# Optimization experiments

Hardware: AMD Instinct MI355X
Metric: run time of the kernel (lower is better)

## Reference

```python
import jax, jax.numpy as jnp
import numpy as np

NEG_SLOPE = 0.2

def gat_conv(x, edge_index, W, a_src, a_dst, b):
    # PyG GATConv, heads=1, eval mode (dropout off), add_self_loops=True
    N = x.shape[0]
    h = x @ W                                   # [N, C]
    loops = jnp.arange(N, dtype=edge_index.dtype)
    src = jnp.concatenate([edge_index[0], loops])
    dst = jnp.concatenate([edge_index[1], loops])
    s_src = h @ a_src                            # [N]
    s_dst = h @ a_dst                            # [N]
    e = s_src[src] + s_dst[dst]                  # [E+N]
    e = jnp.where(e > 0, e, NEG_SLOPE * e)       # leaky_relu
    # segment softmax over destination neighborhoods
    m = jax.ops.segment_max(e, dst, num_segments=N)
    ex = jnp.exp(e - m[dst])
    denom = jax.ops.segment_sum(ex, dst, num_segments=N)
    alpha = ex / denom[dst]                      # [E+N]
    out = jax.ops.segment_sum(alpha[:, None] * h[src], dst, num_segments=N)
    return out + b

def setup_inputs() -> dict:
    key = jax.random.key(0)
    ks = jax.random.split(key, 10)
    N, F_in, H, C, E = 100000, 256, 128, 40, 1600000
    x = jax.random.normal(ks[0], (N, F_in), dtype=jnp.float32)
    edge_index = jax.random.randint(ks[1], (2, E), 0, N, dtype=jnp.int64)
    s1 = 1.0 / np.sqrt(F_in)
    s2 = 1.0 / np.sqrt(H)
    W1 = jax.random.normal(ks[2], (F_in, H), dtype=jnp.float32) * s1
    a_src1 = jax.random.normal(ks[3], (H,), dtype=jnp.float32) * s2
    a_dst1 = jax.random.normal(ks[4], (H,), dtype=jnp.float32) * s2
    b1 = jnp.zeros((H,), dtype=jnp.float32)
    W2 = jax.random.normal(ks[5], (H, C), dtype=jnp.float32) * s2
    a_src2 = jax.random.normal(ks[6], (C,), dtype=jnp.float32) * 0.1
    a_dst2 = jax.random.normal(ks[7], (C,), dtype=jnp.float32) * 0.1
    b2 = jnp.zeros((C,), dtype=jnp.float32)
    return {"x": x, "edge_index": edge_index, "W1": W1, "a_src1": a_src1,
            "a_dst1": a_dst1, "b1": b1, "W2": W2, "a_src2": a_src2,
            "a_dst2": a_dst2, "b2": b2}

def reference(x, edge_index, W1, a_src1, a_dst1, b1, W2, a_src2, a_dst2, b2):
    h = gat_conv(x, edge_index, W1, a_src1, a_dst1, b1)
    h = jax.nn.relu(h)
    # dropout(p=0.6) is identity in eval mode
    h = gat_conv(h, edge_index, W2, a_src2, a_dst2, b2)
    return jax.nn.log_softmax(h, axis=1)
```

## Files before the change

### kernel.cpp

```cpp
#include <hip/hip_runtime.h>
#include <math.h>

#define NEG_SLOPE 0.2f
#define CAP 64
#define NB 64
#define NBUCKET 1563
#define BCAP 1408
#define BINCHUNK 8192
#define NBINB 196

typedef __attribute__((ext_vector_type(8))) short short8;
typedef __attribute__((ext_vector_type(4))) short short4v;
typedef __attribute__((ext_vector_type(4))) float f32x4;
typedef __attribute__((ext_vector_type(2))) float f32x2;

__device__ inline unsigned short f2bf(float f) {
    union { float f; unsigned u; } x; x.f = f;
    unsigned r = x.u + 0x7FFFu + ((x.u >> 16) & 1u);
    return (unsigned short)(r >> 16);
}

__device__ __forceinline__ void gload_lds16(const void* g, void* l) {
    __builtin_amdgcn_global_load_lds(
        (const __attribute__((address_space(1))) void*)g,
        (__attribute__((address_space(3))) void*)l, 16, 0, 0);
}


__global__ __launch_bounds__(256) void init_kernel(
    const float* __restrict__ W1, const float* __restrict__ W2,
    short* __restrict__ bsw1, short* __restrict__ bsw2,
    int* __restrict__ ctrl)
{
    int t = blockIdx.x * 256 + threadIdx.x;
    if (t < 4096) {
        int lane = t & 63;
        int f = t >> 6;
        int k_step = f & 7;
        int n_tile = f >> 3;
        int n  = n_tile * 16 + (lane & 15);
        int k0 = k_step * 32 + (lane >> 4) * 8;
        short8 v;
        #pragma unroll
        for (int j = 0; j < 8; j++)
            v[j] = (short)f2bf(W1[(size_t)(k0 + j) * 128 + n]);
        ((short8*)bsw1)[t] = v;
    } else if (t < 4096 + 768) {
        int u = t - 4096;
        int lane = u & 63;
        int f = u >> 6;
        int k_step = f & 3;
        int n_tile = f >> 2;
        int n  = n_tile * 16 + (lane & 15);
        int k0 = k_step * 32 + (lane >> 4) * 8;
        short8 v;
        #pragma unroll
        for (int j = 0; j < 8; j++)
            v[j] = (n < 40) ? (short)f2bf(W2[(size_t)(k0 + j) * 40 + n]) : (short)0;
        ((short8*)bsw2)[u] = v;
    } else {
        for (int i = t - 4864; i < NBUCKET + 4; i += 256)
            if (i >= 0) ctrl[i] = 0;
    }
}

__global__ __launch_bounds__(256, 2) void k1_kernel(
    const int* __restrict__ ei, int* __restrict__ bcnt,
    unsigned* __restrict__ bbuf, int E,
    const float* __restrict__ x, const short* __restrict__ bsw,
    const float* __restrict__ a_src, const float* __restrict__ a_dst,
    unsigned char* __restrict__ h1, float* __restrict__ s_src,
    float* __restrict__ s_dst, int M)
{
    __shared__ __align__(16) char smem[16896];
    const int tid = threadIdx.x;
    const int bi = blockIdx.x;
    const int q = bi / 9, r = bi - q * 9;

    if (r == 0 && q < NBINB) {
        int* lc = (int*)smem;
        const int base = q * BINCHUNK;
        int n = E - base; if (n > BINCHUNK) n = BINCHUNK;

        for (int b = tid; b < NBUCKET; b += 256) lc[b] = 0;
        __syncthreads();
        for (int i = tid; i < n; i += 256)
            atomicAdd(&lc[ei[E + base + i] >> 6], 1);
        __syncthreads();
        for (int b = tid; b < NBUCKET; b += 256) {
            int c = lc[b];
            lc[b] = c ? atomicAdd(&bcnt[b], c) : 0;
        }
        __syncthreads();
        for (int i = tid; i < n; i += 256) {
            int s = ei[base + i];
            int d = ei[E + base + i];
            int b = d >> 6;
            int pos = atomicAdd(&lc[b], 1);
            if (pos < BCAP)
                bbuf[(size_t)b * BCAP + pos] = (unsigned)s | ((unsigned)(d & 63) << 17);
        }
        return;
    }

    const int nbin = (q < NBINB) ? (q + (r ? 1 : 0)) : NBINB;
    const int vb = bi - nbin;
    const int wave = tid >> 6, lane = tid & 63;
    short8* lbs = (short8*)smem;
    const int rowBase = vb * 64;
    const int arow = rowBase + wave * 16 + (lane & 15);
    const int acol0 = (lane >> 4) * 8;
    const bool rv = (arow < M);
    const float* __restrict__ xr = x + (size_t)arow * 256 + acol0;
    const char* __restrict__ bsb = (const char*)bsw;

    auto stage = [&](int buf, int nt) {
        const char* s = bsb + nt * 8192 + wave * 2048 + lane * 16;
        char* d = smem + buf * 8192 + wave * 2048 + lane * 16;
        gload_lds16(s, d);
        gload_lds16(s + 1024, d + 1024);
    };

    stage(0, 0);

    float4 px[8], qx[8];
    #pragma unroll
    for (int k = 0; k < 8; k++) {
        px[k] = make_float4(0.f, 0.f, 0.f, 0.f);
        qx[k] = px[k];
        if (rv) {
            px[k] = *(const float4*)(xr + k * 32);
            qx[k] = *(const float4*)(xr + k * 32 + 4);
        }
    }
    short8 a[8];
    #pragma unroll
    for (int k = 0; k < 8; k++) {
        short8 t;
        t[0] = (short)f2bf(px[k].x); t[1] = (short)f2bf(px[k].y);
        t[2] = (short)f2bf(px[k].z); t[3] = (short)f2bf(px[k].w);
        t[4] = (short)f2bf(qx[k].x); t[5] = (short)f2bf(qx[k].y);
        t[6] = (short)f2bf(qx[k].z); t[7] = (short)f2bf(qx[k].w);
        a[k] = t;
    }

    const int R0 = rowBase + wave * 16 + (lane >> 4) * 4;
    const int Cb = lane & 15;

    float asv[8], adv[8];
    #pragma unroll
    for (int nt = 0; nt < 8; nt++) {
        asv[nt] = a_src[nt * 16 + Cb];
        adv[nt] = a_dst[nt * 16 + Cb];
    }

    stage(1, 1);

    float ss[4] = {0.f, 0.f, 0.f, 0.f};
    float sd[4] = {0.f, 0.f, 0.f, 0.f};
    f32x4 prev = {0.f, 0.f, 0.f, 0.f};
    int wpk[4][4];

    #pragma unroll
    for (int nt = 0; nt < 8; nt++) {
        if (nt == 7) asm volatile("s_waitcnt vmcnt(0)" ::: "memory");
        else         asm volatile("s_waitcnt vmcnt(2)" ::: "memory");
        __builtin_amdgcn_s_barrier();

        short8 breg[8];
        #pragma unroll
        for (int k = 0; k < 8; k++) breg[k] = lbs[(nt & 1) * 512 + k * 64 + lane];
        asm volatile("s_waitcnt lgkmcnt(0)" ::: "memory");
        __builtin_amdgcn_sched_barrier(0);
        __builtin_amdgcn_s_barrier();

        if (nt < 6) stage(nt & 1, nt + 2);

        __builtin_amdgcn_s_setprio(1);
        f32x4 acc = {0.f, 0.f, 0.f, 0.f};
        #pragma unroll
        for (int k = 0; k < 8; k++)
            acc = __builtin_amdgcn_mfma_f32_16x16x32_bf16(a[k], breg[k], acc, 0, 0, 0);
        __builtin_amdgcn_s_setprio(0);

        float as_ = asv[nt], ad_ = adv[nt];
        #pragma unroll
        for (int r2 = 0; r2 < 4; r2++) {
            float v = acc[r2];
            ss[r2] = fmaf(v, as_, ss[r2]);
            sd[r2] = fmaf(v, ad_, sd[r2]);
        }
        if (nt & 1) {
            #pragma unroll
            for (int r2 = 0; r2 < 4; r2++)
                wpk[nt >> 1][r2] = __builtin_amdgcn_cvt_pk_fp8_f32(prev[r2], acc[r2], 0, false);
        } else {
            prev = acc;
        }
    }

    #pragma unroll
    for (int r2 = 0; r2 < 4; r2++) {
        int R = R0 + r2;
        if (R < M) {
            #pragma unroll
            for (int t = 0; t < 4; t++)
                *(unsigned short*)(h1 + (size_t)R * 128 + t * 32 + 2 * Cb) =
                    (unsigned short)wpk[t][r2];
        }
    }
    #pragma unroll
    for (int off = 1; off < 16; off <<= 1) {
        #pragma unroll
        for (int r2 = 0; r2 < 4; r2++) {
            ss[r2] += __shfl_xor(ss[r2], off);
            sd[r2] += __shfl_xor(sd[r2], off);
        }
    }
    if ((lane & 15) == 0) {
        #pragma unroll
        for (int r2 = 0; r2 < 4; r2++) {
            int R = R0 + r2;
            if (R < M) { s_src[R] = ss[r2]; s_dst[R] = sd[r2]; }
        }
    }
}

__global__ __launch_bounds__(256) void fill_kernel(
    const int* __restrict__ bcnt, const unsigned* __restrict__ bbuf,
    int* __restrict__ csr, int* __restrict__ sorted, int* __restrict__ clsCnt,
    int M)
{
    __shared__ int lcnt[NB];
    __shared__ int lcsr[NB][CAP];
    __shared__ int chist[4];
    __shared__ int cbase[4];
    const int tid = threadIdx.x;
    const int b = blockIdx.x;
    const int nb = b * NB;

    if (tid < NB) lcnt[tid] = 0;
    if (tid < 4) chist[tid] = 0;
    __syncthreads();

    if (tid < NB && nb + tid < M) {
        int pos = atomicAdd(&lcnt[tid], 1);
        if (pos < CAP) lcsr[tid][pos] = nb + tid;
    }

    int ne = bcnt[b]; if (ne > BCAP) ne = BCAP;
    const unsigned* __restrict__ bp = bbuf + (size_t)b * BCAP;
    for (int j = tid; j < ne; j += 256) {
        unsigned v = bp[j];
        int s  = v & 0x1FFFF;
        int dl = v >> 17;
        int pos = atomicAdd(&lcnt[dl], 1);
        if (pos < CAP) lcsr[dl][pos] = s;
    }
    __syncthreads();

    const int4* __restrict__ srcp = (const int4*)&lcsr[0][0];
    int4* __restrict__ dstp = (int4*)(csr + (size_t)nb * CAP);
    #pragma unroll 4
    for (int j = tid; j < NB * CAP / 4; j += 256) dstp[j] = srcp[j];

    int deg = 0, cls = 0, pos = 0;
    bool isNode = (tid < NB && nb + tid < M);
    if (isNode) {
        deg = lcnt[tid]; if (deg > CAP) deg = CAP;
        cls = (deg - 1) >> 4;
        pos = atomicAdd(&chist[cls], 1);
    }
    __syncthreads();
    if (tid < 4) cbase[tid] = chist[tid] ? atomicAdd(&clsCnt[tid], chist[tid]) : 0;
    __syncthreads();
    if (isNode)
        sorted[(size_t)cls * M + cbase[cls] + pos] = (nb + tid) | (deg << 17);
}

__global__ __launch_bounds__(256, 4) void agg1_kernel(
    const unsigned char* __restrict__ h, const int* __restrict__ csr,
    const int* __restrict__ sorted, const int* __restrict__ clsCnt,
    const float* __restrict__ s_src, const float* __restrict__ s_dst,
    const float* __restrict__ bias,
    const short* __restrict__ bsw2,
    const float* __restrict__ a_src2, const float* __restrict__ a_dst2,
    unsigned char* __restrict__ h2, float* __restrict__ ss2,
    float* __restrict__ sd2, int N)
{
    __shared__ short lrow[16][136];
    __shared__ int   lnode[16];
    const int tid = threadIdx.x;
    const int lane = tid & 63;
    const int c = lane & 15;
    const int base = lane & 48;
    const int grp = tid >> 4;
    const int g = blockIdx.x * 16 + grp;

    int c0 = clsCnt[0], c01 = c0 + clsCnt[1], c012 = c01 + clsCnt[2];
    int cls, local;
    if (g < c0)        { cls = 0; local = g; }
    else if (g < c01)  { cls = 1; local = g - c0; }
    else if (g < c012) { cls = 2; local = g - c01; }
    else               { cls = 3; local = g - c012; }

    int ent = sorted[(size_t)cls * N + local];
    int n = ent & 0x1FFFF;
    int deg = ent >> 17;
    const int* __restrict__ edges = csr + (size_t)n * CAP;
    float sdn = s_dst[n];

    int s0 = 0, s1 = 0, s2 = 0, s3 = 0;
    float e0 = -1e30f, e1 = -1e30f, e2 = -1e30f, e3 = -1e30f;
    if (c < deg)      { s0 = edges[c];      e0 = s_src[s0] + sdn; }
    if (c + 16 < deg) { s1 = edges[c + 16]; e1 = s_src[s1] + sdn; }
    if (c + 32 < deg) { s2 = edges[c + 32]; e2 = s_src[s2] + sdn; }
    if (c + 48 < deg) { s3 = edges[c + 48]; e3 = s_src[s3] + sdn; }
    e0 = e0 > 0.f ? e0 : NEG_SLOPE * e0;
    e1 = e1 > 0.f ? e1 : NEG_SLOPE * e1;
    e2 = e2 > 0.f ? e2 : NEG_SLOPE * e2;
    e3 = e3 > 0.f ? e3 : NEG_SLOPE * e3;
    float m = fmaxf(fmaxf(e0, e1), fmaxf(e2, e3));
    #pragma unroll
    for (int off = 1; off < 16; off <<= 1) m = fmaxf(m, __shfl_xor(m, off));
    float w0 = (c < deg)      ? __expf(e0 - m) : 0.f;
    float w1 = (c + 16 < deg) ? __expf(e1 - m) : 0.f;
    float w2 = (c + 32 < deg) ? __expf(e2 - m) : 0.f;
    float w3 = (c + 48 < deg) ? __expf(e3 - m) : 0.f;
    float denom = (w0 + w1) + (w2 + w3);
    #pragma unroll
    for (int off = 1; off < 16; off <<= 1) denom += __shfl_xor(denom, off);
    float inv = 1.0f / denom;

    const uint2* __restrict__ hp = (const uint2*)h;
    f32x2 acc0 = {0.f, 0.f}, acc1 = {0.f, 0.f}, acc2 = {0.f, 0.f}, acc3 = {0.f, 0.f};

#define AGG1_BLK(K, SK, WK)                                                  \
    if (16 * K < deg) {                                                      \
        uint2 u[16];                                                         \
        _Pragma("unroll")                                                    \
        for (int jj = 0; jj < 16; jj++) {                                    \
            int sv = __shfl(SK, base + jj);                                  \
            u[jj] = hp[(size_t)sv * 16 + c];                                 \
        }                                                                    \
        _Pragma("unroll")                                                    \
        for (int jj = 0; jj < 16; jj++) {                                    \
            float wv = __shfl(WK, base + jj);                                \
            f32x2 p;                                                         \
            p = __builtin_amdgcn_cvt_pk_f32_fp8(u[jj].x, false); acc0 += p * wv; \
            p = __builtin_amdgcn_cvt_pk_f32_fp8(u[jj].x, true);  acc1 += p * wv; \
            p = __builtin_amdgcn_cvt_pk_f32_fp8(u[jj].y, false); acc2 += p * wv; \
            p = __builtin_amdgcn_cvt_pk_f32_fp8(u[jj].y, true);  acc3 += p * wv; \
        }                                                                    \
    }
    AGG1_BLK(0, s0, w0)
    AGG1_BLK(1, s1, w1)
    AGG1_BLK(2, s2, w2)
    AGG1_BLK(3, s3, w3)
#undef AGG1_BLK

    int cA = 32 * (c >> 2) + 4 * (c & 3);
    float4 bA = *(const float4*)&bias[cA];
    float4 bB = *(const float4*)&bias[cA + 16];
    float r0 = fmaxf(fmaf(acc0.x, inv, bA.x), 0.f);
    float r1 = fmaxf(fmaf(acc1.x, inv, bA.y), 0.f);
    float r2 = fmaxf(fmaf(acc2.x, inv, bA.z), 0.f);
    float r3 = fmaxf(fmaf(acc3.x, inv, bA.w), 0.f);
    float q0 = fmaxf(fmaf(acc0.y, inv, bB.x), 0.f);
    float q1 = fmaxf(fmaf(acc1.y, inv, bB.y), 0.f);
    float q2 = fmaxf(fmaf(acc2.y, inv, bB.z), 0.f);
    float q3 = fmaxf(fmaf(acc3.y, inv, bB.w), 0.f);
    short4v oA = { (short)f2bf(r0), (short)f2bf(r1), (short)f2bf(r2), (short)f2bf(r3) };
    short4v oB = { (short)f2bf(q0), (short)f2bf(q1), (short)f2bf(q2), (short)f2bf(q3) };
    *(short4v*)&lrow[grp][cA] = oA;
    *(short4v*)&lrow[grp][cA + 16] = oB;
    if (c == 0) lnode[grp] = n;
    __syncthreads();

    if (tid >= 64) return;

    const short8* __restrict__ bs = (const short8*)bsw2;
    short8 a[4];
    #pragma unroll
    for (int k = 0; k < 4; k++)
        a[k] = *(const short8*)&lrow[lane & 15][(lane >> 4) * 8 + k * 32];

    float accs[3][4];
    float ssv[4] = {0.f, 0.f, 0.f, 0.f};
    float sdv[4] = {0.f, 0.f, 0.f, 0.f};

    #pragma unroll
    for (int nt = 0; nt < 3; nt++) {
        f32x4 acc = {0.f, 0.f, 0.f, 0.f};
        #pragma unroll
        for (int k = 0; k < 4; k++) {
            short8 b = bs[(nt * 4 + k) * 64 + lane];
            acc = __builtin_amdgcn_mfma_f32_16x16x32_bf16(a[k], b, acc, 0, 0, 0);
        }
        int C = nt * 16 + c;
        bool valid = (C < 40);
        float as_ = valid ? a_src2[C] : 0.f;
        float ad_ = valid ? a_dst2[C] : 0.f;
        #pragma unroll
        for (int r = 0; r < 4; r++) {
            float v = acc[r];
            accs[nt][r] = v;
            ssv[r] = fmaf(v, as_, ssv[r]);
            sdv[r] = fmaf(v, ad_, sdv[r]);
        }
    }
    #pragma unroll
    for (int r = 0; r < 4; r++) {
        int node = lnode[(lane >> 4) * 4 + r];
        int wA = __builtin_amdgcn_cvt_pk_fp8_f32(accs[0][r], accs[1][r], 0, false);
        int wB = __builtin_amdgcn_cvt_pk_fp8_f32(accs[2][r], 0.f, 0, false);
        *(unsigned short*)(h2 + (size_t)node * 64 + 2 * c) = (unsigned short)wA;
        *(unsigned short*)(h2 + (size_t)node * 64 + 32 + 2 * c) = (unsigned short)wB;
    }
    #pragma unroll
    for (int off = 1; off < 16; off <<= 1) {
        #pragma unroll
        for (int r = 0; r < 4; r++) {
            ssv[r] += __shfl_xor(ssv[r], off);
            sdv[r] += __shfl_xor(sdv[r], off);
        }
    }
    if (c == 0) {
        #pragma unroll
        for (int r = 0; r < 4; r++) {
            int node = lnode[(lane >> 4) * 4 + r];
            ss2[node] = ssv[r];
            sd2[node] = sdv[r];
        }
    }
}

__global__ __launch_bounds__(256, 4) void agg2_kernel(
    const unsigned char* __restrict__ h, const int* __restrict__ csr,
    const int* __restrict__ sorted, const int* __restrict__ clsCnt,
    const float* __restrict__ s_src, const float* __restrict__ s_dst,
    const float* __restrict__ bias, float* __restrict__ out, int N)
{
    const int lane = threadIdx.x & 63;
    const int c = lane & 15;
    const int base = lane & 48;
    const int g = blockIdx.x * 16 + (threadIdx.x >> 4);

    int c0 = clsCnt[0], c01 = c0 + clsCnt[1], c012 = c01 + clsCnt[2];
    int cls, local;
    if (g < c0)        { cls = 0; local = g; }
    else if (g < c01)  { cls = 1; local = g - c0; }
    else if (g < c012) { cls = 2; local = g - c01; }
    else               { cls = 3; local = g - c012; }

    int ent = sorted[(size_t)cls * N + local];
    int n = ent & 0x1FFFF;
    int deg = ent >> 17;
    const int* __restrict__ edges = csr + (size_t)n * CAP;
    float sdn = s_dst[n];

    int s0 = 0, s1 = 0, s2 = 0, s3 = 0;
    float e0 = -1e30f, e1 = -1e30f, e2 = -1e30f, e3 = -1e30f;
    if (c < deg)      { s0 = edges[c];      e0 = s_src[s0] + sdn; }
    if (c + 16 < deg) { s1 = edges[c + 16]; e1 = s_src[s1] + sdn; }
    if (c + 32 < deg) { s2 = edges[c + 32]; e2 = s_src[s2] + sdn; }
    if (c + 48 < deg) { s3 = edges[c + 48]; e3 = s_src[s3] + sdn; }
    e0 = e0 > 0.f ? e0 : NEG_SLOPE * e0;
    e1 = e1 > 0.f ? e1 : NEG_SLOPE * e1;
    e2 = e2 > 0.f ? e2 : NEG_SLOPE * e2;
    e3 = e3 > 0.f ? e3 : NEG_SLOPE * e3;
    float m = fmaxf(fmaxf(e0, e1), fmaxf(e2, e3));
    #pragma unroll
    for (int off = 1; off < 16; off <<= 1) m = fmaxf(m, __shfl_xor(m, off));
    float w0 = (c < deg)      ? __expf(e0 - m) : 0.f;
    float w1 = (c + 16 < deg) ? __expf(e1 - m) : 0.f;
    float w2 = (c + 32 < deg) ? __expf(e2 - m) : 0.f;
    float w3 = (c + 48 < deg) ? __expf(e3 - m) : 0.f;
    float denom = (w0 + w1) + (w2 + w3);
    #pragma unroll
    for (int off = 1; off < 16; off <<= 1) denom += __shfl_xor(denom, off);
    float inv = 1.0f / denom;

    const unsigned* __restrict__ hp = (const unsigned*)h;
    f32x2 acc0 = {0.f, 0.f}, acc1 = {0.f, 0.f};

#define AGG2_BLK(K, SK, WK)                                                  \
    if (16 * K < deg) {                                                      \
        unsigned u[16];                                                      \
        _Pragma("unroll")                                                    \
        for (int jj = 0; jj < 16; jj++) {                                    \
            int sv = __shfl(SK, base + jj);                                  \
            u[jj] = hp[(size_t)sv * 16 + c];                                 \
        }                                                                    \
        _Pragma("unroll")                                                    \
        for (int jj = 0; jj < 16; jj++) {                                    \
            float wv = __shfl(WK, base + jj);                                \
            f32x2 p;                                                         \
            p = __builtin_amdgcn_cvt_pk_f32_fp8(u[jj], false); acc0 += p * wv; \
            p = __builtin_amdgcn_cvt_pk_f32_fp8(u[jj], true);  acc1 += p * wv; \
        }                                                                    \
    }
    AGG2_BLK(0, s0, w0)
    AGG2_BLK(1, s1, w1)
    AGG2_BLK(2, s2, w2)
    AGG2_BLK(3, s3, w3)
#undef AGG2_BLK

    float v0 = -1e30f, v1 = -1e30f, v2 = -1e30f, v3 = -1e30f;
    bool has01 = (c < 8), has0 = (c < 12);
    if (has01) {
        v0 = fmaf(acc0.x, inv, bias[2*c]);
        v1 = fmaf(acc0.y, inv, bias[2*c + 16]);
        v2 = fmaf(acc1.x, inv, bias[2*c + 1]);
        v3 = fmaf(acc1.y, inv, bias[2*c + 17]);
    } else if (has0) {
        v0 = fmaf(acc0.x, inv, bias[2*c + 16]);
        v2 = fmaf(acc1.x, inv, bias[2*c + 17]);
    }

    float mx = fmaxf(fmaxf(v0, v1), fmaxf(v2, v3));
    #pragma unroll
    for (int off = 1; off < 16; off <<= 1) mx = fmaxf(mx, __shfl_xor(mx, off));
    float sum = 0.f;
    if (has01) sum = __expf(v0 - mx) + __expf(v1 - mx) + __expf(v2 - mx) + __expf(v3 - mx);
    else if (has0) sum = __expf(v0 - mx) + __expf(v2 - mx);
    #pragma unroll
    for (int off = 1; off < 16; off <<= 1) sum += __shfl_xor(sum, off);
    float lg = mx + __logf(sum);

    if (has01) {
        *(float2*)&out[(size_t)n * 40 + 2*c]      = make_float2(v0 - lg, v2 - lg);
        *(float2*)&out[(size_t)n * 40 + 2*c + 16] = make_float2(v1 - lg, v3 - lg);
    } else if (has0) {
        *(float2*)&out[(size_t)n * 40 + 2*c + 16] = make_float2(v0 - lg, v2 - lg);
    }
}

extern "C" void kernel_launch(void* const* d_in, const int* in_sizes, int n_in,
                              void* d_out, int out_size, void* d_ws, size_t ws_size,
                              hipStream_t stream)
{
    const float* x      = (const float*)d_in[0];
    const int*   ei     = (const int*)d_in[1];
    const float* W1     = (const float*)d_in[2];
    const float* a_src1 = (const float*)d_in[3];
    const float* a_dst1 = (const float*)d_in[4];
    const float* b1     = (const float*)d_in[5];
    const float* W2     = (const float*)d_in[6];
    const float* a_src2 = (const float*)d_in[7];
    const float* a_dst2 = (const float*)d_in[8];
    const float* b2     = (const float*)d_in[9];
    float* out = (float*)d_out;

    const int N = 100000;
    const int E = 1600000;

    char* ws = (char*)d_ws;
    size_t off = 0;
    auto alloc = [&](size_t bytes) -> void* {
        void* p = ws + off;
        off += (bytes + 255) & ~(size_t)255;
        return p;
    };
    unsigned char*  h1b  = (unsigned char*)alloc((size_t)N * 128);
    unsigned char*  h2b  = (unsigned char*)alloc((size_t)N * 64);
    int*   csr    = (int*)alloc((size_t)NBUCKET * NB * CAP * 4);
    int*   sorted = (int*)alloc((size_t)4 * N * 4);
    float* ss1  = (float*)alloc((size_t)N * 4);
    float* sd1  = (float*)alloc((size_t)N * 4);
    float* ss2  = (float*)alloc((size_t)N * 4);
    float* sd2  = (float*)alloc((size_t)N * 4);
    short* bsw1 = (short*)alloc((size_t)4096 * 8 * 2);
    short* bsw2 = (short*)alloc((size_t)768 * 8 * 2);
    int*   ctrl = (int*)alloc((size_t)(NBUCKET + 4) * 4);
    int*   bcnt   = ctrl;
    int*   clsCnt = ctrl + NBUCKET;
    unsigned* bbuf = (unsigned*)alloc((size_t)NBUCKET * BCAP * 4);

    init_kernel<<<dim3(20), dim3(256), 0, stream>>>(W1, W2, bsw1, bsw2, ctrl);

    k1_kernel<<<dim3(NBINB + (N + 63) / 64), dim3(256), 0, stream>>>(
        ei, bcnt, bbuf, E,
        x, bsw1, a_src1, a_dst1, h1b, ss1, sd1, N);

    fill_kernel<<<dim3(NBUCKET), dim3(256), 0, stream>>>(
        bcnt, bbuf, csr, sorted, clsCnt, N);

    agg1_kernel<<<dim3(N / 16), dim3(256), 0, stream>>>(
        h1b, csr, sorted, clsCnt, ss1, sd1, b1,
        bsw2, a_src2, a_dst2, h2b, ss2, sd2, N);

    agg2_kernel<<<dim3(N / 16), dim3(256), 0, stream>>>(
        h2b, csr, sorted, clsCnt, ss2, sd2, b2, out, N);
}
```

Measured before the change: 340.6 us.

## Replace global-atomic edge bucketing with per-chunk local sort and fuse CSR fill into GEMM

Edge binning now sorts each 2048-edge chunk locally in shared memory, using a block-wide prefix scan. Each chunk writes its per-bucket offsets to a prefix table instead of reserving space in fixed-capacity global buckets with atomics. The CSR fill step is merged into the feature-transform kernel by interleaving fill blocks with GEMM blocks, so the separate fill launch goes away and the fill can overlap with the matrix work. The cost is a ~5 MB prefix table and many small, latency-bound scattered reads per bucket, since each fill block walks all 782 chunk segments. This also removes the old per-bucket capacity cap.

```diff
diff --git a/kernel.cpp b/kernel.cpp
--- a/kernel.cpp
+++ b/kernel.cpp
@@ -5,9 +5,9 @@
 #define CAP 64
 #define NB 64
 #define NBUCKET 1563
-#define BCAP 1408
-#define BINCHUNK 8192
-#define NBINB 196
+#define PSTRIDE 1564
+#define CHUNK 2048
+#define NCHK 782
 
 typedef __attribute__((ext_vector_type(8))) short short8;
 typedef __attribute__((ext_vector_type(4))) short short4v;
@@ -27,46 +27,112 @@
 }
 
 
-__global__ __launch_bounds__(256) void init_kernel(
+__global__ __launch_bounds__(256) void front_kernel(
+    const int* __restrict__ ei, unsigned* __restrict__ bbuf,
+    int* __restrict__ pref, int E,
     const float* __restrict__ W1, const float* __restrict__ W2,
-    short* __restrict__ bsw1, short* __restrict__ bsw2,
-    int* __restrict__ ctrl)
+    short* __restrict__ bsw1, short* __restrict__ bsw2)
 {
-    int t = blockIdx.x * 256 + threadIdx.x;
-    if (t < 4096) {
-        int lane = t & 63;
-        int f = t >> 6;
-        int k_step = f & 7;
-        int n_tile = f >> 3;
-        int n  = n_tile * 16 + (lane & 15);
-        int k0 = k_step * 32 + (lane >> 4) * 8;
-        short8 v;
-        #pragma unroll
-        for (int j = 0; j < 8; j++)
-            v[j] = (short)f2bf(W1[(size_t)(k0 + j) * 128 + n]);
-        ((short8*)bsw1)[t] = v;
-    } else if (t < 4096 + 768) {
-        int u = t - 4096;
-        int lane = u & 63;
-        int f = u >> 6;
-        int k_step = f & 3;
-        int n_tile = f >> 2;
-        int n  = n_tile * 16 + (lane & 15);
-        int k0 = k_step * 32 + (lane >> 4) * 8;
-        short8 v;
-        #pragma unroll
-        for (int j = 0; j < 8; j++)
-            v[j] = (n < 40) ? (short)f2bf(W2[(size_t)(k0 + j) * 40 + n]) : (short)0;
-        ((short8*)bsw2)[u] = v;
+    __shared__ int fsm[PSTRIDE + 2 * CHUNK + 4];
+    const int tid = threadIdx.x;
+
+    if (blockIdx.x < NCHK) {
+        int* lc = fsm;
+        int* ls = fsm + PSTRIDE;
+        int* ld = fsm + PSTRIDE + CHUNK;
+        int* ws = fsm + PSTRIDE + 2 * CHUNK;
+        const int q = blockIdx.x;
+        const int base = q * CHUNK;
+        int n = E - base; if (n > CHUNK) n = CHUNK;
+
+        for (int b = tid; b < NBUCKET; b += 256) lc[b] = 0;
+        __syncthreads();
+        for (int i = tid; i < n; i += 256) {
+            int s = ei[base + i];
+            int d = ei[E + base + i];
+            ls[i] = s;
+            ld[i] = d;
+            atomicAdd(&lc[d >> 6], 1);
+        }
+        __syncthreads();
+
+        const int base0 = tid * 7;
+        int loc[7];
+        int run = 0;
+        #pragma unroll
+        for (int j = 0; j < 7; j++) {
+            int idx = base0 + j;
+            int v = (idx < NBUCKET) ? lc[idx] : 0;
+            loc[j] = run;
+            run += v;
+        }
+        const int lane = tid & 63, w = tid >> 6;
+        int inc = run;
+        #pragma unroll
+        for (int off = 1; off < 64; off <<= 1) {
+            int t2 = __shfl_up(inc, off);
+            if (lane >= off) inc += t2;
+        }
+        if (lane == 63) ws[w] = inc;
+        __syncthreads();
+        int wbase = 0;
+        #pragma unroll
+        for (int i = 0; i < 4; i++) if (i < w) wbase += ws[i];
+        int excl = wbase + inc - run;
+        __syncthreads();
+        int* pr = pref + (size_t)q * PSTRIDE;
+        #pragma unroll
+        for (int j = 0; j < 7; j++) {
+            int idx = base0 + j;
+            if (idx < NBUCKET) {
+                int e = excl + loc[j];
+                pr[idx] = e;
+                lc[idx] = e;
+            }
+        }
+        if (tid == 0) pr[NBUCKET] = n;
+        __syncthreads();
+
+        unsigned* bp = bbuf + (size_t)q * CHUNK;
+        for (int i = tid; i < n; i += 256) {
+            int d = ld[i];
+            int pos = atomicAdd(&lc[d >> 6], 1);
+            bp[pos] = (unsigned)ls[i] | ((unsigned)(d & 63) << 17);
+        }
     } else {
-        for (int i = t - 4864; i < NBUCKET + 4; i += 256)
-            if (i >= 0) ctrl[i] = 0;
+        int t = (blockIdx.x - NCHK) * 256 + tid;
+        if (t < 4096) {
+            int lane = t & 63;
+            int f = t >> 6;
+            int k_step = f & 7;
+            int n_tile = f >> 3;
+            int n  = n_tile * 16 + (lane & 15);
+            int k0 = k_step * 32 + (lane >> 4) * 8;
+            short8 v;
+            #pragma unroll
+            for (int j = 0; j < 8; j++)
+                v[j] = (short)f2bf(W1[(size_t)(k0 + j) * 128 + n]);
+            ((short8*)bsw1)[t] = v;
+        } else if (t < 4096 + 768) {
+            int u = t - 4096;
+            int lane = u & 63;
+            int f = u >> 6;
+            int k_step = f & 3;
+            int n_tile = f >> 2;
+            int n  = n_tile * 16 + (lane & 15);
+            int k0 = k_step * 32 + (lane >> 4) * 8;
+            short8 v;
+            #pragma unroll
+            for (int j = 0; j < 8; j++)
+                v[j] = (n < 40) ? (short)f2bf(W2[(size_t)(k0 + j) * 40 + n]) : (short)0;
+            ((short8*)bsw2)[u] = v;
+        }
     }
 }
 
-__global__ __launch_bounds__(256, 2) void k1_kernel(
-    const int* __restrict__ ei, int* __restrict__ bcnt,
-    unsigned* __restrict__ bbuf, int E,
+__global__ __launch_bounds__(256, 2) void mid_kernel(
+    const unsigned* __restrict__ bbuf, const int* __restrict__ pref,
+    int* __restrict__ csr, int* __restrict__ sorted, int* __restrict__ clsCnt,
     const float* __restrict__ x, const short* __restrict__ bsw,
     const float* __restrict__ a_src, const float* __restrict__ a_dst,
     unsigned char* __restrict__ h1, float* __restrict__ s_src,
@@ -75,36 +141,60 @@
     __shared__ __align__(16) char smem[16896];
     const int tid = threadIdx.x;
     const int bi = blockIdx.x;
-    const int q = bi / 9, r = bi - q * 9;
-
-    if (r == 0 && q < NBINB) {
-        int* lc = (int*)smem;
-        const int base = q * BINCHUNK;
-        int n = E - base; if (n > BINCHUNK) n = BINCHUNK;
-
-        for (int b = tid; b < NBUCKET; b += 256) lc[b] = 0;
-        __syncthreads();
-        for (int i = tid; i < n; i += 256)
-            atomicAdd(&lc[ei[E + base + i] >> 6], 1);
-        __syncthreads();
-        for (int b = tid; b < NBUCKET; b += 256) {
-            int c = lc[b];
-            lc[b] = c ? atomicAdd(&bcnt[b], c) : 0;
-        }
-        __syncthreads();
-        for (int i = tid; i < n; i += 256) {
-            int s = ei[base + i];
-            int d = ei[E + base + i];
-            int b = d >> 6;
-            int pos = atomicAdd(&lc[b], 1);
-            if (pos < BCAP)
-                bbuf[(size_t)b * BCAP + pos] = (unsigned)s | ((unsigned)(d & 63) << 17);
-        }
+    const int vb = bi >> 1;
+
+    if ((bi & 1) == 0) {
+        int* lcnt = (int*)smem;
+        int (*lcsr)[CAP] = (int(*)[CAP])(smem + 256);
+        int* chist = (int*)(smem + 256 + 16384);
+        int* cbase = (int*)(smem + 256 + 16384 + 16);
+
+        const int b = vb;
+        const int nb = b * NB;
+
+        if (tid < NB) lcnt[tid] = 0;
+        if (tid < 4) chist[tid] = 0;
+        __syncthreads();
+
+        if (tid < NB && nb + tid < M) {
+            int pos = atomicAdd(&lcnt[tid], 1);
+            if (pos < CAP) lcsr[tid][pos] = nb + tid;
+        }
+
+        for (int q = tid; q < NCHK; q += 256) {
+            const int* pr = pref + (size_t)q * PSTRIDE + b;
+            int p0 = pr[0];
+            int p1 = pr[1];
+            const unsigned* bp = bbuf + (size_t)q * CHUNK;
+            for (int j = p0; j < p1; j++) {
+                unsigned v = bp[j];
+                int dl = v >> 17;
+                int pos = atomicAdd(&lcnt[dl], 1);
+                if (pos < CAP) lcsr[dl][pos] = v & 0x1FFFF;
+            }
+        }
+        __syncthreads();
+
+        const int4* __restrict__ srcp = (const int4*)&lcsr[0][0];
+        int4* __restrict__ dstp = (int4*)(csr + (size_t)nb * CAP);
+        #pragma unroll 4
+        for (int j = tid; j < NB * CAP / 4; j += 256) dstp[j] = srcp[j];
+
+        int deg = 0, cls = 0, pos = 0;
+        bool isNode = (tid < NB && nb + tid < M);
+        if (isNode) {
+            deg = lcnt[tid]; if (deg > CAP) deg = CAP;
+            cls = (deg - 1) >> 4;
+            pos = atomicAdd(&chist[cls], 1);
+        }
+        __syncthreads();
+        if (tid < 4) cbase[tid] = chist[tid] ? atomicAdd(&clsCnt[tid], chist[tid]) : 0;
+        __syncthreads();
+        if (isNode)
+            sorted[(size_t)cls * M + cbase[cls] + pos] = (nb + tid) | (deg << 17);
         return;
     }
 
-    const int nbin = (q < NBINB) ? (q + (r ? 1 : 0)) : NBINB;
-    const int vb = bi - nbin;
     const int wave = tid >> 6, lane = tid & 63;
     short8* lbs = (short8*)smem;
     const int rowBase = vb * 64;
@@ -224,58 +314,6 @@
             if (R < M) { s_src[R] = ss[r2]; s_dst[R] = sd[r2]; }
         }
     }
-}
-
-__global__ __launch_bounds__(256) void fill_kernel(
-    const int* __restrict__ bcnt, const unsigned* __restrict__ bbuf,
-    int* __restrict__ csr, int* __restrict__ sorted, int* __restrict__ clsCnt,
-    int M)
-{
-    __shared__ int lcnt[NB];
-    __shared__ int lcsr[NB][CAP];
-    __shared__ int chist[4];
-    __shared__ int cbase[4];
-    const int tid = threadIdx.x;
-    const int b = blockIdx.x;
-    const int nb = b * NB;
-
-    if (tid < NB) lcnt[tid] = 0;
-    if (tid < 4) chist[tid] = 0;
-    __syncthreads();
-
-    if (tid < NB && nb + tid < M) {
-        int pos = atomicAdd(&lcnt[tid], 1);
-        if (pos < CAP) lcsr[tid][pos] = nb + tid;
-    }
-
-    int ne = bcnt[b]; if (ne > BCAP) ne = BCAP;
-    const unsigned* __restrict__ bp = bbuf + (size_t)b * BCAP;
-    for (int j = tid; j < ne; j += 256) {
-        unsigned v = bp[j];
-        int s  = v & 0x1FFFF;
-        int dl = v >> 17;
-        int pos = atomicAdd(&lcnt[dl], 1);
-        if (pos < CAP) lcsr[dl][pos] = s;
-    }
-    __syncthreads();
-
-    const int4* __restrict__ srcp = (const int4*)&lcsr[0][0];
-    int4* __restrict__ dstp = (int4*)(csr + (size_t)nb * CAP);
-    #pragma unroll 4
-    for (int j = tid; j < NB * CAP / 4; j += 256) dstp[j] = srcp[j];
-
-    int deg = 0, cls = 0, pos = 0;
-    bool isNode = (tid < NB && nb + tid < M);
-    if (isNode) {
-        deg = lcnt[tid]; if (deg > CAP) deg = CAP;
-        cls = (deg - 1) >> 4;
-        pos = atomicAdd(&chist[cls], 1);
-    }
-    __syncthreads();
-    if (tid < 4) cbase[tid] = chist[tid] ? atomicAdd(&clsCnt[tid], chist[tid]) : 0;
-    __syncthreads();
-    if (isNode)
-        sorted[(size_t)cls * M + cbase[cls] + pos] = (nb + tid) | (deg << 17);
 }
 
 __global__ __launch_bounds__(256, 4) void agg1_kernel(
@@ -572,19 +610,18 @@
     float* sd2  = (float*)alloc((size_t)N * 4);
     short* bsw1 = (short*)alloc((size_t)4096 * 8 * 2);
     short* bsw2 = (short*)alloc((size_t)768 * 8 * 2);
-    int*   ctrl = (int*)alloc((size_t)(NBUCKET + 4) * 4);
-    int*   bcnt   = ctrl;
-    int*   clsCnt = ctrl + NBUCKET;
-    unsigned* bbuf = (unsigned*)alloc((size_t)NBUCKET * BCAP * 4);
-
-    init_kernel<<<dim3(20), dim3(256), 0, stream>>>(W1, W2, bsw1, bsw2, ctrl);
-
-    k1_kernel<<<dim3(NBINB + (N + 63) / 64), dim3(256), 0, stream>>>(
-        ei, bcnt, bbuf, E,
+    int*   clsCnt = (int*)alloc((size_t)4 * 4);
+    unsigned* bbuf = (unsigned*)alloc((size_t)NCHK * CHUNK * 4);
+    int*   pref = (int*)alloc((size_t)NCHK * PSTRIDE * 4);
+
+    hipMemsetAsync(clsCnt, 0, 16, stream);
+
+    front_kernel<<<dim3(NCHK + 19), dim3(256), 0, stream>>>(
+        ei, bbuf, pref, E, W1, W2, bsw1, bsw2);
+
+    mid_kernel<<<dim3(2 * NBUCKET), dim3(256), 0, stream>>>(
+        bbuf, pref, csr, sorted, clsCnt,
         x, bsw1, a_src1, a_dst1, h1b, ss1, sd1, N);
-
-    fill_kernel<<<dim3(NBUCKET), dim3(256), 0, stream>>>(
-        bcnt, bbuf, csr, sorted, clsCnt, N);
 
     agg1_kernel<<<dim3(N / 16), dim3(256), 0, stream>>>(
         h1b, csr, sorted, clsCnt, ss1, sd1, b1,
```

After: 280.9 us. 17.5% less time.
